# Kernel tuning notes

Hardware: AMD Instinct MI355X
Metric: run time of the kernel (lower is better)

The kernel has to match this reference:

```python
import jax, jax.numpy as jnp
import numpy as np

# ---- config (from cfg / InstantNGP defaults) ----
W_IMG, H_IMG = 1024, 1024            # uv_reso_w, uv_reso_h
N_LEVELS = 16                        # standard InstantNGP level count
BASE_RES = 16
FINEST_RES = 1024                    # cfg['finest_level']
F_FEAT = 2                           # features per level
LOG2_T = 19                          # cfg['log2_hashmap_size']
T = 1 << LOG2_T
HIDDEN = 64
PRIMES = np.array([1, 2654435761], dtype=np.uint32)  # 2D spatial-hash primes


def setup_inputs() -> dict:
    key = jax.random.key(0)
    ks = jax.random.split(key, 5)
    d_in = N_LEVELS * F_FEAT
    tables = jax.random.uniform(ks[0], (N_LEVELS, T, F_FEAT), jnp.float32, -1e-4, 1e-4)
    W1 = jax.random.normal(ks[1], (d_in, HIDDEN), jnp.float32) / np.sqrt(d_in)
    b1 = jnp.zeros((HIDDEN,), jnp.float32)
    W2 = jax.random.normal(ks[2], (HIDDEN, HIDDEN), jnp.float32) / np.sqrt(HIDDEN)
    b2 = jnp.zeros((HIDDEN,), jnp.float32)
    W3 = jax.random.normal(ks[3], (HIDDEN, 3), jnp.float32) / np.sqrt(HIDDEN)
    b3 = jnp.zeros((3,), jnp.float32)
    return {"tables": tables, "W1": W1, "b1": b1, "W2": W2, "b2": b2, "W3": W3, "b3": b3}


def _uv_coords():
    # replicate torch.meshgrid(arange(W), arange(H), indexing='xy') -> (H, W)
    xx, yy = jnp.meshgrid(jnp.arange(W_IMG), jnp.arange(H_IMG), indexing='xy')
    x = xx.ravel().astype(jnp.float32) / W_IMG
    y = yy.ravel().astype(jnp.float32) / H_IMG
    return jnp.stack([x, y], axis=1)  # [N, 2]


def _hash_encode(coord, tables):
    # coord: [N,2] in [0,1); tables: [L,T,F]
    growth = np.exp((np.log(FINEST_RES) - np.log(BASE_RES)) / (N_LEVELS - 1))
    res = np.floor(BASE_RES * growth ** np.arange(N_LEVELS)).astype(np.float32)  # [L]
    scaled = coord[None, :, :] * res[:, None, None]          # [L,N,2]
    c0f = jnp.floor(scaled)
    frac = scaled - c0f                                       # [L,N,2]
    c0 = c0f.astype(jnp.uint32)
    corners = jnp.array([[0, 0], [1, 0], [0, 1], [1, 1]], dtype=jnp.uint32)  # [4,2]
    cc = c0[:, :, None, :] + corners[None, None]              # [L,N,4,2]
    idx = (cc[..., 0] * jnp.uint32(PRIMES[0])) ^ (cc[..., 1] * jnp.uint32(PRIMES[1]))
    idx = (idx & jnp.uint32(T - 1)).astype(jnp.int32)         # [L,N,4]
    feats = jax.vmap(lambda tab, i: tab[i])(tables, idx)      # [L,N,4,F] scattered gather
    cf = corners.astype(jnp.float32)                          # [4,2]
    # bilinear weights: prod over dims of (frac if corner bit else 1-frac)
    w = jnp.prod(cf[None, None] * frac[:, :, None, :] +
                 (1.0 - cf[None, None]) * (1.0 - frac[:, :, None, :]), axis=-1)  # [L,N,4]
    feat = jnp.einsum('lnc,lncf->lnf', w, feats)              # [L,N,F]
    return jnp.transpose(feat, (1, 0, 2)).reshape(-1, N_LEVELS * F_FEAT)  # [N, L*F]


def reference(tables, W1, b1, W2, b2, W3, b3):
    coord = _uv_coords()                                      # [N,2]
    enc = _hash_encode(coord, tables)                         # [N,32]
    h = jax.nn.relu(enc @ W1 + b1)
    h = jax.nn.relu(h @ W2 + b2)
    out = h @ W3 + b3                                         # [N,3]
    img = out.reshape(H_IMG, W_IMG, 3).transpose(2, 0, 1)     # [3,H,W]
    return jax.nn.sigmoid(img)[None, ...]                     # [1,3,H,W]
```

## Files before the change

### kernel.cpp

```cpp
#include <hip/hip_runtime.h>
#include <math.h>

#define NLEV   16
#define TSIZE  524288
#define TMASK8 0x3FFFF8u
#define PRIME8 4055616904u
#define NPIX   (1024*1024)

typedef __attribute__((ext_vector_type(8))) short s8v;
typedef __attribute__((ext_vector_type(4))) float f4v;
typedef __attribute__((ext_vector_type(2))) float f2v;

struct ResArr { float r[NLEV]; };
union Frag { unsigned int u[4]; s8v v; };

__device__ __forceinline__ unsigned short bf16_rn(float x) {
    unsigned int u = __builtin_bit_cast(unsigned int, x);
    u += 0x7fffu + ((u >> 16) & 1u);
    return (unsigned short)(u >> 16);
}
__device__ __forceinline__ unsigned int pk_bf16(float lo, float hi) {
    return __builtin_amdgcn_perm(__builtin_bit_cast(unsigned int, hi),
                                 __builtin_bit_cast(unsigned int, lo),
                                 0x07060302u);
}

__global__ __launch_bounds__(256) void prep_kernel(
    const float* __restrict__ W1, const float* __restrict__ W2,
    const float* __restrict__ W3, float* __restrict__ ws, ResArr res)
{
    const int t = threadIdx.x;
    if (t < NLEV) ws[t] = res.r[t];
    unsigned short* w1t = (unsigned short*)(ws + 16);
    unsigned short* w2t = w1t + 64 * 32;
    unsigned short* w3t = w2t + 64 * 64;
    for (int i = t; i < 64 * 32; i += 256) {
        int n = i >> 5, k = i & 31;
        w1t[i] = bf16_rn(W1[k * 64 + n]);
    }
    for (int i = t; i < 64 * 64; i += 256) {
        int n2 = i >> 6, kp = i & 63;
        int klog = (kp & 32) | ((kp & 4) << 2) | ((kp & 24) >> 1) | (kp & 3);
        w2t[i] = bf16_rn(W2[klog * 64 + n2]);
    }
    for (int i = t; i < 16 * 64; i += 256) {
        int row = i >> 6, kp = i & 63;
        int klog = (kp & 32) | ((kp & 4) << 2) | ((kp & 24) >> 1) | (kp & 3);
        int ch = row & 3;
        w3t[i] = (ch < 3) ? bf16_rn(W3[klog * 3 + ch]) : (unsigned short)0;
    }
}

__global__ __launch_bounds__(256) void ngp_fused_kernel(
    const float* __restrict__ tables,
    const float* __restrict__ b1, const float* __restrict__ b2,
    const float* __restrict__ b3,
    const float* __restrict__ ws, float* __restrict__ out)
{
    const int tid  = threadIdx.x;
    const int lane = tid & 63;
    const int wv   = tid >> 6;
    const int c15  = lane & 15;
    const int g    = lane >> 4;
    const int xb   = blockIdx.x * 16;
    const int yb   = blockIdx.y * 16;

    const float4 rv = *(const float4*)(ws + g * 4);
    const float rr[4] = { rv.x, rv.y, rv.z, rv.w };
    const float xs = (float)(xb + c15) * (1.0f / 1024.0f);
    float yf[4];
    #pragma unroll
    for (int pt = 0; pt < 4; ++pt)
        yf[pt] = (float)(yb + wv * 4 + pt) * (1.0f / 1024.0f);

    const char* __restrict__ tb = (const char*)tables;
    const unsigned int lvlb = (unsigned int)(g * 4) << 22;

    Frag bfrag[4];
    #pragma unroll
    for (int j = 0; j < 4; ++j) {
        const float r   = rr[j];
        const float sx  = xs * r;
        const float fx0 = floorf(sx);
        const float fx  = sx - fx0;
        const f2v  fx2  = { fx, fx };
        const unsigned int cx8  = ((unsigned int)(int)fx0) << 3;
        const unsigned int cx8b = cx8 + 8u;
        const unsigned int lb   = lvlb + ((unsigned int)j << 22);
        #pragma unroll
        for (int pt = 0; pt < 4; ++pt) {
            const float sy  = yf[pt] * r;
            const float fy0 = floorf(sy);
            const float fy  = sy - fy0;
            const f2v  fy2  = { fy, fy };
            const unsigned int cy  = (unsigned int)(int)fy0;
            const unsigned int hy0 = cy * PRIME8;
            const unsigned int hy1 = hy0 + PRIME8;
            const f2v c00 = *(const f2v*)(tb + (((cx8  ^ hy0) & TMASK8) | lb));
            const f2v c10 = *(const f2v*)(tb + (((cx8b ^ hy0) & TMASK8) | lb));
            const f2v c01 = *(const f2v*)(tb + (((cx8  ^ hy1) & TMASK8) | lb));
            const f2v c11 = *(const f2v*)(tb + (((cx8b ^ hy1) & TMASK8) | lb));
            const f2v top = c00 + fx2 * (c10 - c00);
            const f2v bot = c01 + fx2 * (c11 - c01);
            const f2v e   = top + fy2 * (bot - top);
            bfrag[pt].u[j] = pk_bf16(e[0], e[1]);
        }
    }

    const unsigned short* __restrict__ w1t = (const unsigned short*)(ws + 16);
    const unsigned short* __restrict__ w2t = w1t + 64 * 32;
    const unsigned short* __restrict__ w3t = w2t + 64 * 64;
    const f4v zero4 = { 0.f, 0.f, 0.f, 0.f };

    Frag hp2[2][4];
    #pragma unroll
    for (int mt = 0; mt < 4; ++mt) {
        Frag afr;
        afr.v = *(const s8v*)(w1t + (mt * 16 + c15) * 32 + g * 8);
        const f4v bb = *(const f4v*)(b1 + mt * 16 + g * 4);
        #pragma unroll
        for (int pt = 0; pt < 4; ++pt) {
            f4v acc = zero4;
            acc = __builtin_amdgcn_mfma_f32_16x16x32_bf16(
                afr.v, bfrag[pt].v, acc, 0, 0, 0);
            const f4v hv = __builtin_elementwise_max(acc + bb, zero4);
            hp2[mt >> 1][pt].u[(mt & 1) * 2 + 0] = pk_bf16(hv[0], hv[1]);
            hp2[mt >> 1][pt].u[(mt & 1) * 2 + 1] = pk_bf16(hv[2], hv[3]);
        }
    }

    Frag hq2[2][4];
    #pragma unroll
    for (int mt = 0; mt < 4; ++mt) {
        const f4v bb2 = *(const f4v*)(b2 + mt * 16 + g * 4);
        f4v acc[4] = { zero4, zero4, zero4, zero4 };
        #pragma unroll
        for (int st = 0; st < 2; ++st) {
            Frag a2;
            a2.v = *(const s8v*)(w2t + (mt * 16 + c15) * 64 + st * 32 + g * 8);
            #pragma unroll
            for (int pt = 0; pt < 4; ++pt)
                acc[pt] = __builtin_amdgcn_mfma_f32_16x16x32_bf16(
                    a2.v, hp2[st][pt].v, acc[pt], 0, 0, 0);
        }
        #pragma unroll
        for (int pt = 0; pt < 4; ++pt) {
            const f4v hv = __builtin_elementwise_max(acc[pt] + bb2, zero4);
            hq2[mt >> 1][pt].u[(mt & 1) * 2 + 0] = pk_bf16(hv[0], hv[1]);
            hq2[mt >> 1][pt].u[(mt & 1) * 2 + 1] = pk_bf16(hv[2], hv[3]);
        }
    }

    f4v acc3[4] = { zero4, zero4, zero4, zero4 };
    #pragma unroll
    for (int st = 0; st < 2; ++st) {
        Frag a3;
        a3.v = *(const s8v*)(w3t + c15 * 64 + st * 32 + g * 8);
        #pragma unroll
        for (int pt = 0; pt < 4; ++pt)
            acc3[pt] = __builtin_amdgcn_mfma_f32_16x16x32_bf16(
                a3.v, hq2[st][pt].v, acc3[pt], 0, 0, 0);
    }

    float ov[3];
    #pragma unroll
    for (int c = 0; c < 3; ++c) {
        float v = acc3[0][c];
        v = (g == 1) ? acc3[1][c] : v;
        v = (g == 2) ? acc3[2][c] : v;
        v = (g == 3) ? acc3[3][c] : v;
        ov[c] = v + b3[c];
    }
    const int pix = ((yb + wv * 4 + g) << 10) + xb + c15;
    out[0 * NPIX + pix] = 1.0f / (1.0f + __expf(-ov[0]));
    out[1 * NPIX + pix] = 1.0f / (1.0f + __expf(-ov[1]));
    out[2 * NPIX + pix] = 1.0f / (1.0f + __expf(-ov[2]));
}

extern "C" void kernel_launch(void* const* d_in, const int* in_sizes, int n_in,
                              void* d_out, int out_size, void* d_ws, size_t ws_size,
                              hipStream_t stream) {
    const float* tables = (const float*)d_in[0];
    const float* W1     = (const float*)d_in[1];
    const float* b1     = (const float*)d_in[2];
    const float* W2     = (const float*)d_in[3];
    const float* b2     = (const float*)d_in[4];
    const float* W3     = (const float*)d_in[5];
    const float* b3     = (const float*)d_in[6];
    float* out          = (float*)d_out;
    float* ws           = (float*)d_ws;

    ResArr res;
    const double growth = exp((log(1024.0) - log(16.0)) / 15.0);
    for (int l = 0; l < NLEV; ++l)
        res.r[l] = (float)floor(16.0 * pow(growth, (double)l));

    hipLaunchKernelGGL(prep_kernel, dim3(1), dim3(256), 0, stream, W1, W2, W3, ws, res);
    hipLaunchKernelGGL(ngp_fused_kernel, dim3(64, 64), dim3(256), 0, stream,
                       tables, b1, b2, b3, ws, out);
}
```

Measured before the change: 68.02 us.

## Stage per-block hash-grid corner features in LDS before interpolation

Each 16x16 pixel block now cooperatively gathers the unique grid corners it needs at every level (908 entries in total) into shared memory, using a precomputed index map built in the prep kernel. The bilinear interpolation then reads its four corners from LDS instead of issuing four scattered global loads per level per pixel. This targets redundant global gathers, since neighbouring pixels share corners at the coarse levels. It costs one block-wide barrier, about 7KB of LDS per block, and a fixed per-level corner-window width that has to cover the block's footprint at that resolution.

```diff
diff --git a/kernel.cpp b/kernel.cpp
--- a/kernel.cpp
+++ b/kernel.cpp
@@ -3,9 +3,10 @@
 
 #define NLEV   16
 #define TSIZE  524288
-#define TMASK8 0x3FFFF8u
-#define PRIME8 4055616904u
+#define TMASK  524287
 #define NPIX   (1024*1024)
+#define NCORN  908
+#define MAP_F_OFF 3600
 
 typedef __attribute__((ext_vector_type(8))) short s8v;
 typedef __attribute__((ext_vector_type(4))) float f4v;
@@ -13,6 +14,10 @@
 
 struct ResArr { float r[NLEV]; };
 union Frag { unsigned int u[4]; s8v v; };
+
+#define WC0 3
+#define WC_LIST  {3,3,3,3,3,3,4,4,5,5,6,7,9,11,14,17}
+#define OFF_LIST {0,9,18,27,36,45,54,70,86,111,136,172,221,302,423,619}
 
 __device__ __forceinline__ unsigned short bf16_rn(float x) {
     unsigned int u = __builtin_bit_cast(unsigned int, x);
@@ -34,6 +39,7 @@
     unsigned short* w1t = (unsigned short*)(ws + 16);
     unsigned short* w2t = w1t + 64 * 32;
     unsigned short* w3t = w2t + 64 * 64;
+    unsigned int*   map = (unsigned int*)(ws + MAP_F_OFF);
     for (int i = t; i < 64 * 32; i += 256) {
         int n = i >> 5, k = i & 31;
         w1t[i] = bf16_rn(W1[k * 64 + n]);
@@ -48,6 +54,19 @@
         int klog = (kp & 32) | ((kp & 4) << 2) | ((kp & 24) >> 1) | (kp & 3);
         int ch = row & 3;
         w3t[i] = (ch < 3) ? bf16_rn(W3[klog * 3 + ch]) : (unsigned short)0;
+    }
+    constexpr int WCc[16]  = WC_LIST;
+    constexpr int OFFc[16] = OFF_LIST;
+    for (int i = t; i < NCORN; i += 256) {
+        int l = 0, off = 0, wc = WC0;
+        #pragma unroll
+        for (int k = 1; k < 16; ++k)
+            if (i >= OFFc[k]) { l = k; off = OFFc[k]; wc = WCc[k]; }
+        const int loc = i - off;
+        const int jj  = loc / wc;
+        const int ii  = loc - jj * wc;
+        map[i] = ((unsigned int)l << 16) | ((unsigned int)jj << 8)
+               | (unsigned int)ii;
     }
 }
 
@@ -57,6 +76,8 @@
     const float* __restrict__ b3,
     const float* __restrict__ ws, float* __restrict__ out)
 {
+    __shared__ float2 ldsc[NCORN];
+
     const int tid  = threadIdx.x;
     const int lane = tid & 63;
     const int wv   = tid >> 6;
@@ -65,6 +86,29 @@
     const int xb   = blockIdx.x * 16;
     const int yb   = blockIdx.y * 16;
 
+    const float xbf = (float)xb * (1.0f / 1024.0f);
+    const float ybf = (float)yb * (1.0f / 1024.0f);
+
+    {
+        const unsigned int* __restrict__ map =
+            (const unsigned int*)(ws + MAP_F_OFF);
+        const float2* __restrict__ tabs = (const float2*)tables;
+        for (int i = tid; i < NCORN; i += 256) {
+            const unsigned int m = map[i];
+            const int l  = (int)(m >> 16);
+            const int jj = (int)((m >> 8) & 255u);
+            const int ii = (int)(m & 255u);
+            const float r = ws[l];
+            const int cx0 = (int)floorf(xbf * r);
+            const int cy0 = (int)floorf(ybf * r);
+            const unsigned int idx =
+                (((unsigned int)(cx0 + ii)) ^
+                 ((unsigned int)(cy0 + jj) * 2654435761u)) & TMASK;
+            ldsc[i] = tabs[((size_t)l << 19) + idx];
+        }
+    }
+    __syncthreads();
+
     const float4 rv = *(const float4*)(ws + g * 4);
     const float rr[4] = { rv.x, rv.y, rv.z, rv.w };
     const float xs = (float)(xb + c15) * (1.0f / 1024.0f);
@@ -73,33 +117,35 @@
     for (int pt = 0; pt < 4; ++pt)
         yf[pt] = (float)(yb + wv * 4 + pt) * (1.0f / 1024.0f);
 
-    const char* __restrict__ tb = (const char*)tables;
-    const unsigned int lvlb = (unsigned int)(g * 4) << 22;
-
+    constexpr int WCc[16]  = WC_LIST;
+    constexpr int OFFc[16] = OFF_LIST;
     Frag bfrag[4];
     #pragma unroll
     for (int j = 0; j < 4; ++j) {
+        int wc  = WCc[j];      int off = OFFc[j];
+        wc  = (g == 1) ? WCc[4 + j]  : wc;  off = (g == 1) ? OFFc[4 + j]  : off;
+        wc  = (g == 2) ? WCc[8 + j]  : wc;  off = (g == 2) ? OFFc[8 + j]  : off;
+        wc  = (g == 3) ? WCc[12 + j] : wc;  off = (g == 3) ? OFFc[12 + j] : off;
         const float r   = rr[j];
         const float sx  = xs * r;
         const float fx0 = floorf(sx);
         const float fx  = sx - fx0;
         const f2v  fx2  = { fx, fx };
-        const unsigned int cx8  = ((unsigned int)(int)fx0) << 3;
-        const unsigned int cx8b = cx8 + 8u;
-        const unsigned int lb   = lvlb + ((unsigned int)j << 22);
+        const int ii    = (int)fx0 - (int)floorf(xbf * r);
+        const int cy0i  = (int)floorf(ybf * r);
+        const int rowb  = off + ii;
         #pragma unroll
         for (int pt = 0; pt < 4; ++pt) {
             const float sy  = yf[pt] * r;
             const float fy0 = floorf(sy);
             const float fy  = sy - fy0;
             const f2v  fy2  = { fy, fy };
-            const unsigned int cy  = (unsigned int)(int)fy0;
-            const unsigned int hy0 = cy * PRIME8;
-            const unsigned int hy1 = hy0 + PRIME8;
-            const f2v c00 = *(const f2v*)(tb + (((cx8  ^ hy0) & TMASK8) | lb));
-            const f2v c10 = *(const f2v*)(tb + (((cx8b ^ hy0) & TMASK8) | lb));
-            const f2v c01 = *(const f2v*)(tb + (((cx8  ^ hy1) & TMASK8) | lb));
-            const f2v c11 = *(const f2v*)(tb + (((cx8b ^ hy1) & TMASK8) | lb));
+            const int jj    = (int)fy0 - cy0i;
+            const int base  = rowb + jj * wc;
+            const f2v c00 = *(const f2v*)&ldsc[base];
+            const f2v c10 = *(const f2v*)&ldsc[base + 1];
+            const f2v c01 = *(const f2v*)&ldsc[base + wc];
+            const f2v c11 = *(const f2v*)&ldsc[base + wc + 1];
             const f2v top = c00 + fx2 * (c10 - c00);
             const f2v bot = c01 + fx2 * (c11 - c01);
             const f2v e   = top + fy2 * (bot - top);
```

Measured after the change: 70.11 us. 1.03x slower.
